# Optimization experiments

Hardware: AMD Instinct MI355X
Metric: run time of the kernel (lower is better)

Reference implementation:

```python
import jax, jax.numpy as jnp
import numpy as np
import math

N_QUBITS = 8
N_QLAYERS = 2
NUM_HEADS = 2


def run_circuit(x, weights):
    """Simulate PennyLane circuit: AngleEmbedding(RX) + BasicEntanglerLayers(RX + CNOT ring),
    measure <Z_i> on every wire.  x: (T, n) real angles, weights: (L, n) real angles.
    Returns (T, n) expectation values."""
    T, n = x.shape
    L = weights.shape[0]
    # AngleEmbedding: product state prod_q RX(x_q)|0> = [cos(x/2), -i sin(x/2)]
    half = 0.5 * x
    amps = jnp.stack([jnp.cos(half).astype(jnp.complex64),
                      (-1j) * jnp.sin(half).astype(jnp.complex64)], axis=-1)  # (T, n, 2)
    state = amps[:, 0, :]  # (T, 2)
    for q in range(1, n):
        state = (state[:, :, None] * amps[:, q][:, None, :]).reshape(T, -1)
    state = state.reshape((T,) + (2,) * n)  # qubit 0 = axis 1 (most significant)

    for l in range(L):
        cl = jnp.cos(0.5 * weights[l]).astype(jnp.complex64)
        sl = jnp.sin(0.5 * weights[l]).astype(jnp.complex64)
        # RX(weights[l, q]) on each wire (shared angle across tokens)
        for q in range(n):
            s0 = jnp.take(state, 0, axis=1 + q)
            s1 = jnp.take(state, 1, axis=1 + q)
            n0 = cl[q] * s0 - 1j * sl[q] * s1
            n1 = -1j * sl[q] * s0 + cl[q] * s1
            state = jnp.stack([n0, n1], axis=1 + q)
        # CNOT ring: control q -> target (q+1) % n
        for q in range(n):
            ctrl, tgt = q, (q + 1) % n
            s0 = jnp.take(state, 0, axis=1 + ctrl)
            s1 = jnp.take(state, 1, axis=1 + ctrl)
            t_axis = 1 + tgt - (1 if tgt > ctrl else 0)  # target axis after removing ctrl axis
            s1 = jnp.flip(s1, axis=t_axis)
            state = jnp.stack([s0, s1], axis=1 + ctrl)

    probs = (state.real ** 2 + state.imag ** 2).reshape(T, 2 ** n)
    # <Z_q> = sum_idx probs[idx] * (1 - 2*bit_q(idx)); qubit 0 is MSB
    idx = np.arange(2 ** n)
    bits = (idx[None, :] >> np.arange(n - 1, -1, -1)[:, None]) & 1  # (n, 2^n)
    signs = jnp.asarray(1 - 2 * bits, dtype=probs.dtype)
    return probs @ signs.T  # (T, n)


def setup_inputs() -> dict:
    key = jax.random.key(0)
    kx, kq, kk, kv, kc = jax.random.split(key, 5)
    B, S, E = 32, 1024, N_QUBITS
    two_pi = 2.0 * math.pi
    return {
        "x": jax.random.normal(kx, (B, S, E), dtype=jnp.float32),
        "wq": jax.random.uniform(kq, (N_QLAYERS, N_QUBITS), dtype=jnp.float32) * two_pi,
        "wk": jax.random.uniform(kk, (N_QLAYERS, N_QUBITS), dtype=jnp.float32) * two_pi,
        "wv": jax.random.uniform(kv, (N_QLAYERS, N_QUBITS), dtype=jnp.float32) * two_pi,
        "wc": jax.random.uniform(kc, (N_QLAYERS, N_QUBITS), dtype=jnp.float32) * two_pi,
    }


def reference(x, wq, wk, wv, wc):
    B, S, E = x.shape
    H = NUM_HEADS
    d_k = E // H
    tok = x.reshape(B * S, E)
    Q = run_circuit(tok, wq).reshape(B, S, H, d_k).transpose(0, 2, 1, 3)  # (B,H,S,d)
    K = run_circuit(tok, wk).reshape(B, S, H, d_k).transpose(0, 2, 1, 3)
    V = run_circuit(tok, wv).reshape(B, S, H, d_k).transpose(0, 2, 1, 3)
    scores = jnp.einsum('bhqd,bhkd->bhqk', Q, K) / jnp.sqrt(jnp.asarray(d_k, x.dtype))
    attn = jax.nn.softmax(scores, axis=-1)  # dropout is identity in eval mode
    ctx = jnp.einsum('bhqk,bhkd->bhqd', attn, V)  # (B,H,S,d)
    ctx = ctx.transpose(0, 2, 1, 3).reshape(B, S, E)
    out = run_circuit(ctx.reshape(B * S, E), wc).reshape(B, S, E)
    return out
```

## Files before the change

kernel.cpp:

```cpp
#include <hip/hip_runtime.h>

#define TT 32768
#define S_LEN 1024
#define KC 16

__device__ __align__(16) float g_Q[TT * 8];
__device__ __align__(16) float g_K[TT * 8];
__device__ __align__(16) float g_V[TT * 8];
__device__ __align__(16) float4 gp_acc[KC * 64 * 1024];
__device__ float gp_den[KC * 64 * 1024];
__device__ float g_coef[4][8][128];

struct PTerm { unsigned ymask, zonly, tmask; float sgn; };
struct OTab { PTerm t[128]; int n; unsigned amask; };

constexpr unsigned conjZring(unsigned a) {
    for (int q = 7; q >= 0; --q) {
        const int c = q, tt = (q + 1) & 7;
        if ((a >> tt) & 1u) a ^= (1u << c);
    }
    return a;
}
constexpr unsigned conjXring(unsigned b) {
    for (int q = 7; q >= 0; --q) {
        const int c = q, tt = (q + 1) & 7;
        if ((b >> c) & 1u) b ^= (1u << tt);
    }
    return b;
}
constexpr int popc8(unsigned v) { int n = 0; for (int i = 0; i < 8; ++i) n += (v >> i) & 1; return n; }

constexpr OTab build_tab(int i) {
    OTab o{};
    o.n = 0;
    const unsigned a1 = conjZring(1u << i);
    o.amask = a1;
    const unsigned a3 = conjZring(a1);
    unsigned T = a1;
    while (true) {
        const unsigned b3 = conjXring(T);
        if (!(b3 & ~a3)) {
            const int k = popc8(T) + popc8(b3);
            const int idx = (k & 1) ? 100000 : o.n;
            o.t[idx].ymask = b3;
            o.t[idx].zonly = a3 & ~b3;
            o.t[idx].tmask = T;
            o.t[idx].sgn = ((k >> 1) & 1) ? -1.f : 1.f;
            o.n++;
        }
        if (T == 0) break;
        T = (T - 1) & a1;
    }
    return o;
}

constexpr OTab g_tab[8] = {build_tab(0), build_tab(1), build_tab(2), build_tab(3),
                           build_tab(4), build_tab(5), build_tab(6), build_tab(7)};
static_assert(g_tab[0].n >= 1 && g_tab[0].n <= 128, "term count");
static_assert(g_tab[7].n >= 1 && g_tab[7].n <= 128, "term count");

template <int I>
__device__ __forceinline__ void coef_one(const float s1[8], const float c1[8], float* dst)
{
    constexpr OTab tb = g_tab[I];
#pragma unroll
    for (int k = 0; k < tb.n; ++k) {
        float c = tb.t[k].sgn;
#pragma unroll
        for (int q = 0; q < 8; ++q) {
            if ((tb.t[k].tmask >> q) & 1) c *= s1[q];
            else if ((tb.amask >> q) & 1) c *= c1[q];
        }
        dst[k] = c;
    }
}

__global__ __launch_bounds__(64) void precoef(
    const float* __restrict__ wq, const float* __restrict__ wk,
    const float* __restrict__ wv, const float* __restrict__ wc)
{
    int tid = threadIdx.x;
    if (tid >= 32) return;
    int set = tid >> 3, i = tid & 7;
    const float* w = (set == 0) ? wq : (set == 1) ? wk : (set == 2) ? wv : wc;
    float s1[8], c1[8];
#pragma unroll
    for (int q = 0; q < 8; ++q) __sincosf(w[8 + q], &s1[q], &c1[q]);
    float* dst = &g_coef[set][i][0];
    switch (i) {
        case 0: coef_one<0>(s1, c1, dst); break;
        case 1: coef_one<1>(s1, c1, dst); break;
        case 2: coef_one<2>(s1, c1, dst); break;
        case 3: coef_one<3>(s1, c1, dst); break;
        case 4: coef_one<4>(s1, c1, dst); break;
        case 5: coef_one<5>(s1, c1, dst); break;
        case 6: coef_one<6>(s1, c1, dst); break;
        case 7: coef_one<7>(s1, c1, dst); break;
    }
}

template <int I>
__device__ __forceinline__ float eval_out(const float cs[8], const float sn[8],
                                          const float* __restrict__ coefI)
{
    constexpr OTab tb = g_tab[I];
    float acc = 0.f;
#pragma unroll
    for (int k = 0; k < tb.n; ++k) {
        float p = coefI[k];
#pragma unroll
        for (int q = 0; q < 8; ++q) {
            if ((tb.t[k].ymask >> q) & 1) p *= sn[q];
            else if ((tb.t[k].zonly >> q) & 1) p *= cs[q];
        }
        acc += p;
    }
    return acc;
}

__device__ __forceinline__ void eval_all(const float th[8],
                                         const float (*__restrict__ coef)[128],
                                         float ev[8])
{
    float cs[8], sn[8];
#pragma unroll
    for (int q = 0; q < 8; ++q) __sincosf(th[q], &sn[q], &cs[q]);
    ev[0] = eval_out<0>(cs, sn, coef[0]);
    ev[1] = eval_out<1>(cs, sn, coef[1]);
    ev[2] = eval_out<2>(cs, sn, coef[2]);
    ev[3] = eval_out<3>(cs, sn, coef[3]);
    ev[4] = eval_out<4>(cs, sn, coef[4]);
    ev[5] = eval_out<5>(cs, sn, coef[5]);
    ev[6] = eval_out<6>(cs, sn, coef[6]);
    ev[7] = eval_out<7>(cs, sn, coef[7]);
}

#define QSCALE 0.72134752044448170368f

__device__ __forceinline__ float fexp2(float s)
{
    float r;
    asm("v_exp_f32 %0, %1" : "=v"(r) : "v"(s));
    return r;
}

__global__ __launch_bounds__(256) void qkv_pauli(
    const float* __restrict__ x, const float* __restrict__ wq,
    const float* __restrict__ wk, const float* __restrict__ wv)
{
    int t = blockIdx.x * 256 + threadIdx.x;
    int set = blockIdx.y;
    const float* w = (set == 0) ? wq : (set == 1) ? wk : wv;
    float* out = (set == 0) ? g_Q : (set == 1) ? g_K : g_V;
    float4 xa = ((const float4*)x)[t * 2];
    float4 xb = ((const float4*)x)[t * 2 + 1];
    float th[8] = {xa.x + w[0], xa.y + w[1], xa.z + w[2], xa.w + w[3],
                   xb.x + w[4], xb.y + w[5], xb.z + w[6], xb.w + w[7]};
    float ev[8];
    eval_all(th, g_coef[set], ev);
    float sc = (set == 0) ? QSCALE : 1.f;
#pragma unroll
    for (int i = 0; i < 8; ++i) ev[i] *= sc;
    ((float4*)out)[t * 2]     = make_float4(ev[0], ev[1], ev[2], ev[3]);
    ((float4*)out)[t * 2 + 1] = make_float4(ev[4], ev[5], ev[6], ev[7]);
}

__global__ __launch_bounds__(128, 2) void attn_part()
{
    __shared__ float4 Ks[64];
    __shared__ float4 Vs[64];
    int bh = blockIdx.x, kc = blockIdx.y;
    int b = bh >> 1, h = bh & 1;
    int tid = threadIdx.x;

    const float* Qb = g_Q + (size_t)b * S_LEN * 8 + h * 4;
    float4 qv[8];
#pragma unroll
    for (int c = 0; c < 8; ++c)
        qv[c] = *(const float4*)(Qb + (size_t)(tid + c * 128) * 8);

    size_t rowbase = (size_t)b * S_LEN + kc * 64;
    if (tid < 64) {
        Ks[tid] = *(const float4*)(g_K + (rowbase + tid) * 8 + h * 4);
    } else {
        int r = tid - 64;
        Vs[r] = *(const float4*)(g_V + (rowbase + r) * 8 + h * 4);
    }
    __syncthreads();

    float den[8];
    float4 ac[8];
#pragma unroll
    for (int c = 0; c < 8; ++c) {
        den[c] = 0.f;
        ac[c] = make_float4(0.f, 0.f, 0.f, 0.f);
    }
#pragma unroll 2
    for (int k = 0; k < 64; ++k) {
        float4 kk = Ks[k];
        float4 vv = Vs[k];
#pragma unroll
        for (int c = 0; c < 8; ++c) {
            float s = qv[c].x * kk.x + qv[c].y * kk.y + qv[c].z * kk.z + qv[c].w * kk.w;
            float e = fexp2(s);
            den[c] += e;
            ac[c].x += e * vv.x; ac[c].y += e * vv.y;
            ac[c].z += e * vv.z; ac[c].w += e * vv.w;
        }
    }
    int base = kc * 65536 + bh * 1024 + tid;
#pragma unroll
    for (int c = 0; c < 8; ++c) {
        gp_acc[base + c * 128] = ac[c];
        gp_den[base + c * 128] = den[c];
    }
}

__global__ __launch_bounds__(256) void outc_pauli(
    const float* __restrict__ wc, float* __restrict__ out)
{
    int t = blockIdx.x * 256 + threadIdx.x;
    int b = t >> 10, s = t & 1023;
    float th[8];
#pragma unroll
    for (int h = 0; h < 2; ++h) {
        float4 A = make_float4(0.f, 0.f, 0.f, 0.f);
        float D = 0.f;
#pragma unroll
        for (int kc = 0; kc < KC; ++kc) {
            int idx = kc * 65536 + (b * 2 + h) * 1024 + s;
            float4 a = gp_acc[idx];
            A.x += a.x; A.y += a.y; A.z += a.z; A.w += a.w;
            D += gp_den[idx];
        }
        float inv = 1.f / D;
        th[h * 4 + 0] = A.x * inv + wc[h * 4 + 0];
        th[h * 4 + 1] = A.y * inv + wc[h * 4 + 1];
        th[h * 4 + 2] = A.z * inv + wc[h * 4 + 2];
        th[h * 4 + 3] = A.w * inv + wc[h * 4 + 3];
    }
    float ev[8];
    eval_all(th, g_coef[3], ev);
    ((float4*)out)[t * 2]     = make_float4(ev[0], ev[1], ev[2], ev[3]);
    ((float4*)out)[t * 2 + 1] = make_float4(ev[4], ev[5], ev[6], ev[7]);
}

extern "C" void kernel_launch(void* const* d_in, const int* in_sizes, int n_in,
                              void* d_out, int out_size, void* d_ws, size_t ws_size,
                              hipStream_t stream)
{
    const float* x  = (const float*)d_in[0];
    const float* wq = (const float*)d_in[1];
    const float* wk = (const float*)d_in[2];
    const float* wv = (const float*)d_in[3];
    const float* wc = (const float*)d_in[4];

    precoef<<<1, 64, 0, stream>>>(wq, wk, wv, wc);
    qkv_pauli<<<dim3(TT / 256, 3), 256, 0, stream>>>(x, wq, wk, wv);
    attn_part<<<dim3(64, KC), 128, 0, stream>>>();
    outc_pauli<<<TT / 256, 256, 0, stream>>>(wc, (float*)d_out);
}
```

Baseline: 49.93 us.

## Compute attention with bf16 MFMA and drop split-K partial reduction

The scalar-FMA attention, which split keys into 16 chunks and wrote partials to global memory, is replaced by a per-wave MFMA kernel. It computes QK^T and P·V with 32x32x16 bf16 MFMAs and gets the softmax denominator from a ones row folded into the V operand. Q, K and a transposed V are stored as zero-padded bf16, so the output kernel no longer reads and reduces 16 partial sums. The change trades fp32 accuracy for bf16 scores and probabilities, and each wave now loops over all 32 key blocks serially.

```diff
diff --git a/kernel.cpp b/kernel.cpp
--- a/kernel.cpp
+++ b/kernel.cpp
@@ -2,13 +2,14 @@
 
 #define TT 32768
 #define S_LEN 1024
-#define KC 16
-
-__device__ __align__(16) float g_Q[TT * 8];
-__device__ __align__(16) float g_K[TT * 8];
-__device__ __align__(16) float g_V[TT * 8];
-__device__ __align__(16) float4 gp_acc[KC * 64 * 1024];
-__device__ float gp_den[KC * 64 * 1024];
+
+typedef __attribute__((ext_vector_type(8))) short short8;
+typedef __attribute__((ext_vector_type(16))) float f32x16;
+
+__device__ __align__(16) short g_Qb[64 * 1024 * 8];
+__device__ __align__(16) short g_Kb[64 * 1024 * 8];
+__device__ __align__(16) short g_Vt[64 * 4 * 1024];
+__device__ __align__(16) float g_C[TT * 8];
 __device__ float g_coef[4][8][128];
 
 struct PTerm { unsigned ymask, zonly, tmask; float sgn; };
@@ -144,6 +145,13 @@
     return r;
 }
 
+__device__ __forceinline__ short f2bf(float f)
+{
+    unsigned u = __float_as_uint(f);
+    unsigned r = (u + 0x7FFFu + ((u >> 16) & 1u)) >> 16;
+    return (short)r;
+}
+
 __global__ __launch_bounds__(256) void qkv_pauli(
     const float* __restrict__ x, const float* __restrict__ wq,
     const float* __restrict__ wk, const float* __restrict__ wv)
@@ -151,68 +159,110 @@
     int t = blockIdx.x * 256 + threadIdx.x;
     int set = blockIdx.y;
     const float* w = (set == 0) ? wq : (set == 1) ? wk : wv;
-    float* out = (set == 0) ? g_Q : (set == 1) ? g_K : g_V;
     float4 xa = ((const float4*)x)[t * 2];
     float4 xb = ((const float4*)x)[t * 2 + 1];
     float th[8] = {xa.x + w[0], xa.y + w[1], xa.z + w[2], xa.w + w[3],
                    xb.x + w[4], xb.y + w[5], xb.z + w[6], xb.w + w[7]};
     float ev[8];
     eval_all(th, g_coef[set], ev);
-    float sc = (set == 0) ? QSCALE : 1.f;
-#pragma unroll
-    for (int i = 0; i < 8; ++i) ev[i] *= sc;
-    ((float4*)out)[t * 2]     = make_float4(ev[0], ev[1], ev[2], ev[3]);
-    ((float4*)out)[t * 2 + 1] = make_float4(ev[4], ev[5], ev[6], ev[7]);
-}
-
-__global__ __launch_bounds__(128, 2) void attn_part()
-{
-    __shared__ float4 Ks[64];
-    __shared__ float4 Vs[64];
-    int bh = blockIdx.x, kc = blockIdx.y;
-    int b = bh >> 1, h = bh & 1;
-    int tid = threadIdx.x;
-
-    const float* Qb = g_Q + (size_t)b * S_LEN * 8 + h * 4;
-    float4 qv[8];
-#pragma unroll
-    for (int c = 0; c < 8; ++c)
-        qv[c] = *(const float4*)(Qb + (size_t)(tid + c * 128) * 8);
-
-    size_t rowbase = (size_t)b * S_LEN + kc * 64;
-    if (tid < 64) {
-        Ks[tid] = *(const float4*)(g_K + (rowbase + tid) * 8 + h * 4);
+
+    int b = t >> 10, s = t & 1023;
+    if (set == 2) {
+#pragma unroll
+        for (int h = 0; h < 2; ++h)
+#pragma unroll
+            for (int d = 0; d < 4; ++d)
+                g_Vt[((size_t)((b * 2 + h) * 4 + d)) * 1024 + s] = f2bf(ev[h * 4 + d]);
     } else {
-        int r = tid - 64;
-        Vs[r] = *(const float4*)(g_V + (rowbase + r) * 8 + h * 4);
-    }
-    __syncthreads();
-
-    float den[8];
-    float4 ac[8];
-#pragma unroll
-    for (int c = 0; c < 8; ++c) {
-        den[c] = 0.f;
-        ac[c] = make_float4(0.f, 0.f, 0.f, 0.f);
-    }
-#pragma unroll 2
-    for (int k = 0; k < 64; ++k) {
-        float4 kk = Ks[k];
-        float4 vv = Vs[k];
-#pragma unroll
-        for (int c = 0; c < 8; ++c) {
-            float s = qv[c].x * kk.x + qv[c].y * kk.y + qv[c].z * kk.z + qv[c].w * kk.w;
-            float e = fexp2(s);
-            den[c] += e;
-            ac[c].x += e * vv.x; ac[c].y += e * vv.y;
-            ac[c].z += e * vv.z; ac[c].w += e * vv.w;
-        }
-    }
-    int base = kc * 65536 + bh * 1024 + tid;
-#pragma unroll
-    for (int c = 0; c < 8; ++c) {
-        gp_acc[base + c * 128] = ac[c];
-        gp_den[base + c * 128] = den[c];
+        short* dst = (set == 0) ? g_Qb : g_Kb;
+        float sc = (set == 0) ? QSCALE : 1.f;
+#pragma unroll
+        for (int h = 0; h < 2; ++h) {
+            short8 row;
+            row[0] = f2bf(ev[h * 4 + 0] * sc);
+            row[1] = f2bf(ev[h * 4 + 1] * sc);
+            row[2] = f2bf(ev[h * 4 + 2] * sc);
+            row[3] = f2bf(ev[h * 4 + 3] * sc);
+            row[4] = 0; row[5] = 0; row[6] = 0; row[7] = 0;
+            *(short8*)(dst + ((size_t)(b * 2 + h) * 1024 + s) * 8) = row;
+        }
+    }
+}
+
+__global__ __launch_bounds__(256) void attn_mfma()
+{
+    int lane = threadIdx.x & 63;
+    int gw = blockIdx.x * 4 + (threadIdx.x >> 6);
+    int bh = gw >> 5, qblk = gw & 31;
+    int l31 = lane & 31, hi = lane >> 5;
+
+    short8 zero8 = {0, 0, 0, 0, 0, 0, 0, 0};
+    short8 ones8 = {0x3F80, 0x3F80, 0x3F80, 0x3F80, 0x3F80, 0x3F80, 0x3F80, 0x3F80};
+
+    short8 qf = zero8;
+    if (lane < 32)
+        qf = *(const short8*)(g_Qb + ((size_t)bh * 1024 + qblk * 32 + l31) * 8);
+
+    f32x16 acc;
+#pragma unroll
+    for (int r = 0; r < 16; ++r) acc[r] = 0.f;
+
+    for (int kc = 0; kc < 32; ++kc) {
+        short8 kf = zero8;
+        if (lane < 32)
+            kf = *(const short8*)(g_Kb + ((size_t)bh * 1024 + kc * 32 + l31) * 8);
+
+        f32x16 zc;
+#pragma unroll
+        for (int r = 0; r < 16; ++r) zc[r] = 0.f;
+        f32x16 c1 = __builtin_amdgcn_mfma_f32_32x32x16_bf16(kf, qf, zc, 0, 0, 0);
+
+        float p[16];
+#pragma unroll
+        for (int r = 0; r < 16; ++r) p[r] = fexp2(c1[r]);
+
+        unsigned w0, w1, w2, w3, w4, w5, w6, w7;
+        asm("v_cvt_pk_bf16_f32 %0, %1, %2" : "=v"(w0) : "v"(p[0]),  "v"(p[1]));
+        asm("v_cvt_pk_bf16_f32 %0, %1, %2" : "=v"(w1) : "v"(p[2]),  "v"(p[3]));
+        asm("v_cvt_pk_bf16_f32 %0, %1, %2" : "=v"(w2) : "v"(p[4]),  "v"(p[5]));
+        asm("v_cvt_pk_bf16_f32 %0, %1, %2" : "=v"(w3) : "v"(p[6]),  "v"(p[7]));
+        asm("v_cvt_pk_bf16_f32 %0, %1, %2" : "=v"(w4) : "v"(p[8]),  "v"(p[9]));
+        asm("v_cvt_pk_bf16_f32 %0, %1, %2" : "=v"(w5) : "v"(p[10]), "v"(p[11]));
+        asm("v_cvt_pk_bf16_f32 %0, %1, %2" : "=v"(w6) : "v"(p[12]), "v"(p[13]));
+        asm("v_cvt_pk_bf16_f32 %0, %1, %2" : "=v"(w7) : "v"(p[14]), "v"(p[15]));
+        asm("v_permlane32_swap_b32 %0, %1" : "+v"(w0), "+v"(w2));
+        asm("v_permlane32_swap_b32 %0, %1" : "+v"(w1), "+v"(w3));
+        asm("v_permlane32_swap_b32 %0, %1" : "+v"(w4), "+v"(w6));
+        asm("v_permlane32_swap_b32 %0, %1" : "+v"(w5), "+v"(w7));
+
+        union { unsigned u[4]; short8 s8; } ba, bb;
+        ba.u[0] = w0; ba.u[1] = w1; ba.u[2] = w2; ba.u[3] = w3;
+        bb.u[0] = w4; bb.u[1] = w5; bb.u[2] = w6; bb.u[3] = w7;
+
+        short8 va = zero8, vb = zero8;
+        if (l31 < 4) {
+            const short* vp = g_Vt + ((size_t)bh * 4 + l31) * 1024 + kc * 32 + hi * 8;
+            va = *(const short8*)(vp);
+            vb = *(const short8*)(vp + 16);
+        } else if (l31 == 4) {
+            va = ones8;
+            vb = ones8;
+        }
+        acc = __builtin_amdgcn_mfma_f32_32x32x16_bf16(va, ba.s8, acc, 0, 0, 0);
+        acc = __builtin_amdgcn_mfma_f32_32x32x16_bf16(vb, bb.s8, acc, 0, 0, 0);
+    }
+
+    float t0 = acc[0], t1 = acc[0];
+    asm("v_permlane32_swap_b32 %0, %1" : "+v"(t0), "+v"(t1));
+    float den = t0 + t1 - acc[0];
+    if (lane < 32) {
+        float inv = 1.f / den;
+        int b = bh >> 1, h = bh & 1;
+        float* cp = g_C + ((size_t)b * 1024 + qblk * 32 + l31) * 8 + h * 4;
+        cp[0] = acc[0] * inv;
+        cp[1] = acc[1] * inv;
+        cp[2] = acc[2] * inv;
+        cp[3] = acc[3] * inv;
     }
 }
 
@@ -220,25 +270,10 @@
     const float* __restrict__ wc, float* __restrict__ out)
 {
     int t = blockIdx.x * 256 + threadIdx.x;
-    int b = t >> 10, s = t & 1023;
-    float th[8];
-#pragma unroll
-    for (int h = 0; h < 2; ++h) {
-        float4 A = make_float4(0.f, 0.f, 0.f, 0.f);
-        float D = 0.f;
-#pragma unroll
-        for (int kc = 0; kc < KC; ++kc) {
-            int idx = kc * 65536 + (b * 2 + h) * 1024 + s;
-            float4 a = gp_acc[idx];
-            A.x += a.x; A.y += a.y; A.z += a.z; A.w += a.w;
-            D += gp_den[idx];
-        }
-        float inv = 1.f / D;
-        th[h * 4 + 0] = A.x * inv + wc[h * 4 + 0];
-        th[h * 4 + 1] = A.y * inv + wc[h * 4 + 1];
-        th[h * 4 + 2] = A.z * inv + wc[h * 4 + 2];
-        th[h * 4 + 3] = A.w * inv + wc[h * 4 + 3];
-    }
+    float4 ca = ((const float4*)g_C)[t * 2];
+    float4 cb = ((const float4*)g_C)[t * 2 + 1];
+    float th[8] = {ca.x + wc[0], ca.y + wc[1], ca.z + wc[2], ca.w + wc[3],
+                   cb.x + wc[4], cb.y + wc[5], cb.z + wc[6], cb.w + wc[7]};
     float ev[8];
     eval_all(th, g_coef[3], ev);
     ((float4*)out)[t * 2]     = make_float4(ev[0], ev[1], ev[2], ev[3]);
@@ -257,6 +292,6 @@
 
     precoef<<<1, 64, 0, stream>>>(wq, wk, wv, wc);
     qkv_pauli<<<dim3(TT / 256, 3), 256, 0, stream>>>(x, wq, wk, wv);
-    attn_part<<<dim3(64, KC), 128, 0, stream>>>();
+    attn_mfma<<<512, 256, 0, stream>>>();
     outc_pauli<<<TT / 256, 256, 0, stream>>>(wc, (float*)d_out);
 }
```

Result: faster. 45.81 us (-8.3%).
